# Optimization experiments

Measured on AMD Instinct MI355X. Metric: run time of the kernel, lower is better.

The kernel has to match this reference:

```python
import jax, jax.numpy as jnp
from jax import lax
import numpy as np

T, B, NIN, H, NOUT = 256, 64, 512, 512, 512


def _lstm_dir(x, w_ih, w_hh, b_ih, b_hh, reverse):
    # x: [T,B,NIN]; w_ih: [4H,NIN]; w_hh: [4H,H]
    xg = jnp.einsum('tbi,gi->tbg', x, w_ih) + b_ih + b_hh  # [T,B,4H]
    if reverse:
        xg = xg[::-1]
    h0 = jnp.zeros((x.shape[1], w_hh.shape[1]), x.dtype)

    def step(carry, g):
        h, c = carry
        g = g + h @ w_hh.T
        i, f, gg, o = jnp.split(g, 4, axis=-1)  # PyTorch gate order i,f,g,o
        i = jax.nn.sigmoid(i)
        f = jax.nn.sigmoid(f)
        gg = jnp.tanh(gg)
        o = jax.nn.sigmoid(o)
        c = f * c + i * gg
        h = o * jnp.tanh(c)
        return (h, c), h

    _, hs = lax.scan(step, (h0, h0), xg)
    if reverse:
        hs = hs[::-1]
    return hs  # [T,B,H]


def setup_inputs() -> dict:
    key = jax.random.key(0)
    ks = jax.random.split(key, 12)
    s_in = 1.0 / np.sqrt(H)
    u = lambda k, shape: jax.random.uniform(k, shape, jnp.float32, -s_in, s_in)
    return {
        'x': jax.random.normal(ks[0], (T, B, NIN), jnp.float32),
        'w_ih_f': u(ks[1], (4 * H, NIN)),
        'w_hh_f': u(ks[2], (4 * H, H)),
        'b_ih_f': u(ks[3], (4 * H,)),
        'b_hh_f': u(ks[4], (4 * H,)),
        'w_ih_b': u(ks[5], (4 * H, NIN)),
        'w_hh_b': u(ks[6], (4 * H, H)),
        'b_ih_b': u(ks[7], (4 * H,)),
        'b_hh_b': u(ks[8], (4 * H,)),
        'fc_w': u(ks[9], (NOUT, 2 * H)),
        'fc_b': u(ks[10], (NOUT,)),
    }


def reference(x, w_ih_f, w_hh_f, b_ih_f, b_hh_f, w_ih_b, w_hh_b, b_ih_b, b_hh_b, fc_w, fc_b):
    h_f = _lstm_dir(x, w_ih_f, w_hh_f, b_ih_f, b_hh_f, reverse=False)
    h_b = _lstm_dir(x, w_ih_b, w_hh_b, b_ih_b, b_hh_b, reverse=True)
    h = jnp.concatenate([h_f, h_b], axis=-1)  # [T,B,2H]
    out = jnp.einsum('tbh,oh->tbo', h, fc_w) + fc_b  # fused linear over T*B rows
    return out
```

## Files before the change

kernel.cpp:

```cpp
#include <hip/hip_runtime.h>

typedef unsigned short u16;
typedef short v8s __attribute__((ext_vector_type(8)));
typedef float v4f __attribute__((ext_vector_type(4)));

#define TT 256
#define BB 64
#define HH 512
#define G4 2048
#define MTB 16384

static __device__ __forceinline__ float bf2f(u16 u) {
    unsigned int x = ((unsigned int)u) << 16;
    union { unsigned int i; float f; } c; c.i = x; return c.f;
}
static __device__ __forceinline__ u16 f2bf(float f) {
    union { float f; unsigned int i; } c; c.f = f;
    unsigned int u = c.i;
    u += 0x7fffu + ((u >> 16) & 1u);
    return (u16)(u >> 16);
}

__global__ __launch_bounds__(256) void cvt_bf16(const float* __restrict__ src,
                                                u16* __restrict__ dst, int n) {
    int i = blockIdx.x * blockDim.x + threadIdx.x;
    int stride = gridDim.x * blockDim.x;
    for (int j = i * 4; j < n; j += stride * 4) {
        float4 v = *reinterpret_cast<const float4*>(src + j);
        ushort4 o;
        o.x = f2bf(v.x); o.y = f2bf(v.y); o.z = f2bf(v.z); o.w = f2bf(v.w);
        *reinterpret_cast<ushort4*>(dst + j) = o;
    }
}

template<bool OUT_BF16, bool BIAS_M>
__global__ __launch_bounds__(256) void gemm_bt(const u16* __restrict__ A,
                                               const u16* __restrict__ Bm,
                                               void* __restrict__ Cv,
                                               const float* __restrict__ bias1,
                                               const float* __restrict__ bias2,
                                               int M, int N, int K) {
    __shared__ u16 lds_a[128 * 64];
    __shared__ u16 lds_b[128 * 64];
    const int tid = threadIdx.x, lane = tid & 63;
    const int m0 = blockIdx.y * 128, n0 = blockIdx.x * 128;
    const int wid = tid >> 6, wm = wid >> 1, wn = wid & 1;
    v4f acc[4][4] = {};

    const int srow  = tid >> 3;
    const int skoff = (tid & 7) * 8;
    const u16* Ag = A + (size_t)(m0 + srow) * K + skoff;
    const u16* Bg = Bm + (size_t)(n0 + srow) * K + skoff;
    u16* la = lds_a + srow * 64 + skoff;
    u16* lb = lds_b + srow * 64 + skoff;

    for (int k0 = 0; k0 < K; k0 += 64) {
        #pragma unroll
        for (int q = 0; q < 4; ++q) {
            *reinterpret_cast<v8s*>(la + q * 32 * 64) =
                *reinterpret_cast<const v8s*>(Ag + (size_t)q * 32 * K + k0);
            *reinterpret_cast<v8s*>(lb + q * 32 * 64) =
                *reinterpret_cast<const v8s*>(Bg + (size_t)q * 32 * K + k0);
        }
        __syncthreads();
        #pragma unroll
        for (int kk = 0; kk < 2; ++kk) {
            v8s af[4], bfr[4];
            #pragma unroll
            for (int i = 0; i < 4; ++i)
                af[i] = *reinterpret_cast<const v8s*>(
                    lds_a + (wm * 64 + i * 16 + (lane & 15)) * 64 + kk * 32 + (lane >> 4) * 8);
            #pragma unroll
            for (int i = 0; i < 4; ++i)
                bfr[i] = *reinterpret_cast<const v8s*>(
                    lds_b + (wn * 64 + i * 16 + (lane & 15)) * 64 + kk * 32 + (lane >> 4) * 8);
            #pragma unroll
            for (int i = 0; i < 4; ++i)
                #pragma unroll
                for (int j = 0; j < 4; ++j)
                    acc[i][j] = __builtin_amdgcn_mfma_f32_16x16x32_bf16(af[i], bfr[j], acc[i][j], 0, 0, 0);
        }
        __syncthreads();
    }
    #pragma unroll
    for (int i = 0; i < 4; ++i) {
        #pragma unroll
        for (int j = 0; j < 4; ++j) {
            #pragma unroll
            for (int r = 0; r < 4; ++r) {
                int m = m0 + wm * 64 + i * 16 + (lane >> 4) * 4 + r;
                int n = n0 + wn * 64 + j * 16 + (lane & 15);
                float v = acc[i][j][r];
                if (BIAS_M) { v += bias1[m]; if (bias2) v += bias2[m]; }
                else        { v += bias1[n]; }
                if (OUT_BF16) ((u16*)Cv)[(size_t)m * N + n] = f2bf(v);
                else          ((float*)Cv)[(size_t)m * N + n] = v;
            }
        }
    }
}

static __device__ __forceinline__ float sigm(float x) { return 1.f / (1.f + __expf(-x)); }
static __device__ __forceinline__ float tanh_(float x) { return 2.f / (1.f + __expf(-2.f * x)) - 1.f; }

__global__ __launch_bounds__(256, 2) void lstm_persist(
    const u16* __restrict__ w_hh,
    const u16* __restrict__ xgT,
    u16* __restrict__ h_all,
    unsigned* __restrict__ flags)
{
    __shared__ u16 wlds[4 * 16 * 64 * 8];
    const int bx = blockIdx.x;
    const int d = bx >> 5, cg = bx & 31;
    const int lane = threadIdx.x & 63, nf = threadIdx.x >> 6;
    const int lrow = lane & 15, lk = lane >> 4;
    const int b = nf * 16 + lrow;

    {
        const int G = nf;
        const u16* wrow = w_hh + ((size_t)d * G4 + G * HH + cg * 16 + lrow) * HH + lk * 8;
        #pragma unroll
        for (int kk = 0; kk < 16; ++kk)
            *reinterpret_cast<v8s*>(&wlds[((G * 16 + kk) * 64 + lane) * 8]) =
                *reinterpret_cast<const v8s*>(wrow + kk * 32);
    }
    __syncthreads();

    float c[4] = {0.f, 0.f, 0.f, 0.f};
    float xg[4][4];
    unsigned* fl = flags + (d * 4 + nf) * 32;

    {
        const int t0 = d ? (TT - 1) : 0;
        const u16* xgb = xgT + (size_t)d * G4 * MTB + (size_t)t0 * BB + b;
        #pragma unroll
        for (int G = 0; G < 4; ++G)
            #pragma unroll
            for (int r = 0; r < 4; ++r)
                xg[G][r] = bf2f(xgb[(size_t)(G * HH + cg * 16 + lk * 4 + r) * MTB]);
    }

    for (int s = 0; s < TT; ++s) {
        const int t = d ? (TT - 1 - s) : s;
        v4f acc[4] = {};
        if (s > 0) {
            v8s af0[4][4];
            #pragma unroll
            for (int G = 0; G < 4; ++G)
                #pragma unroll
                for (int kk = 0; kk < 4; ++kk)
                    af0[G][kk] = *reinterpret_cast<const v8s*>(
                        &wlds[((G * 16 + kk) * 64 + lane) * 8]);
            const unsigned tgt = (unsigned)s;
            while (true) {
                unsigned fv = __hip_atomic_load(&fl[lane & 31],
                                                __ATOMIC_RELAXED, __HIP_MEMORY_SCOPE_AGENT);
                if (__all((int)(fv >= tgt))) break;
            }
            asm volatile("" ::: "memory");
            const int tprev = d ? (t + 1) : (t - 1);
            const u16* hp = h_all + ((size_t)tprev * BB + b) * 1024 + d * HH + lk * 8;
            v8s bf_[16];
            #pragma unroll
            for (int kk = 0; kk < 16; ++kk) {
                union { unsigned long long w[2]; v8s v; } u;
                const u16* p = hp + kk * 32;
                u.w[0] = __hip_atomic_load((const unsigned long long*)p,
                                           __ATOMIC_RELAXED, __HIP_MEMORY_SCOPE_AGENT);
                u.w[1] = __hip_atomic_load((const unsigned long long*)(p + 4),
                                           __ATOMIC_RELAXED, __HIP_MEMORY_SCOPE_AGENT);
                bf_[kk] = u.v;
            }
            #pragma unroll
            for (int kk = 0; kk < 4; ++kk)
                #pragma unroll
                for (int G = 0; G < 4; ++G)
                    acc[G] = __builtin_amdgcn_mfma_f32_16x16x32_bf16(af0[G][kk], bf_[kk], acc[G], 0, 0, 0);
            #pragma unroll
            for (int kk = 4; kk < 16; ++kk)
                #pragma unroll
                for (int G = 0; G < 4; ++G) {
                    v8s af = *reinterpret_cast<const v8s*>(
                        &wlds[((G * 16 + kk) * 64 + lane) * 8]);
                    acc[G] = __builtin_amdgcn_mfma_f32_16x16x32_bf16(af, bf_[kk], acc[G], 0, 0, 0);
                }
        }
        ushort4 hout;
        #pragma unroll
        for (int r = 0; r < 4; ++r) {
            float pi = acc[0][r] + xg[0][r];
            float pf = acc[1][r] + xg[1][r];
            float pg = acc[2][r] + xg[2][r];
            float po = acc[3][r] + xg[3][r];
            float iv = sigm(pi), fv = sigm(pf), gv = tanh_(pg), ov = sigm(po);
            float cc = fv * c[r] + iv * gv;
            c[r] = cc;
            ((u16*)&hout)[r] = f2bf(ov * tanh_(cc));
        }
        union { ushort4 v; unsigned long long q; } hu; hu.v = hout;
        __hip_atomic_store((unsigned long long*)(
                h_all + ((size_t)t * BB + b) * 1024 + d * HH + cg * 16 + lk * 4),
            hu.q, __ATOMIC_RELAXED, __HIP_MEMORY_SCOPE_AGENT);
        asm volatile("s_waitcnt vmcnt(0)" ::: "memory");
        if (lane == 0)
            __hip_atomic_store(&fl[cg], (unsigned)(s + 1),
                               __ATOMIC_RELAXED, __HIP_MEMORY_SCOPE_AGENT);
        if (s + 1 < TT) {
            const int tn = d ? (TT - 2 - s) : (s + 1);
            const u16* xgb = xgT + (size_t)d * G4 * MTB + (size_t)tn * BB + b;
            #pragma unroll
            for (int G = 0; G < 4; ++G)
                #pragma unroll
                for (int r = 0; r < 4; ++r)
                    xg[G][r] = bf2f(xgb[(size_t)(G * HH + cg * 16 + lk * 4 + r) * MTB]);
        }
    }
}

extern "C" void kernel_launch(void* const* d_in, const int* in_sizes, int n_in,
                              void* d_out, int out_size, void* d_ws, size_t ws_size,
                              hipStream_t stream) {
    const float* x    = (const float*)d_in[0];
    const float* wihf = (const float*)d_in[1];
    const float* whhf = (const float*)d_in[2];
    const float* bihf = (const float*)d_in[3];
    const float* bhhf = (const float*)d_in[4];
    const float* wihb = (const float*)d_in[5];
    const float* whhb = (const float*)d_in[6];
    const float* bihb = (const float*)d_in[7];
    const float* bhhb = (const float*)d_in[8];
    const float* fcw  = (const float*)d_in[9];
    const float* fcb  = (const float*)d_in[10];

    char* ws = (char*)d_ws;
    size_t off = 0;
    auto alloc = [&](size_t bytes) {
        off = (off + 255) & ~(size_t)255;
        char* p = ws + off; off += bytes; return p;
    };
    u16* x_bf    = (u16*)alloc((size_t)MTB * 512 * 2);
    u16* wih_bf  = (u16*)alloc((size_t)2 * G4 * 512 * 2);
    u16* whh_bf  = (u16*)alloc((size_t)2 * G4 * 512 * 2);
    u16* fcw_bf  = (u16*)alloc((size_t)512 * 1024 * 2);
    u16* xgT     = (u16*)alloc((size_t)2 * G4 * MTB * 2);
    u16* h_all   = (u16*)alloc((size_t)MTB * 1024 * 2);
    unsigned* flags = (unsigned*)alloc(2 * 4 * 32 * sizeof(unsigned));
    (void)ws_size;

    cvt_bf16<<<1024, 256, 0, stream>>>(x, x_bf, MTB * 512);
    cvt_bf16<<<256, 256, 0, stream>>>(wihf, wih_bf, G4 * 512);
    cvt_bf16<<<256, 256, 0, stream>>>(wihb, wih_bf + (size_t)G4 * 512, G4 * 512);
    cvt_bf16<<<256, 256, 0, stream>>>(whhf, whh_bf, G4 * 512);
    cvt_bf16<<<256, 256, 0, stream>>>(whhb, whh_bf + (size_t)G4 * 512, G4 * 512);
    cvt_bf16<<<128, 256, 0, stream>>>(fcw, fcw_bf, 512 * 1024);

    gemm_bt<true, true><<<dim3(MTB / 128, G4 / 128), 256, 0, stream>>>(
        wih_bf, x_bf, xgT, bihf, bhhf, G4, MTB, 512);
    gemm_bt<true, true><<<dim3(MTB / 128, G4 / 128), 256, 0, stream>>>(
        wih_bf + (size_t)G4 * 512, x_bf, xgT + (size_t)G4 * MTB, bihb, bhhb, G4, MTB, 512);

    hipMemsetAsync(flags, 0, 2 * 4 * 32 * sizeof(unsigned), stream);
    lstm_persist<<<64, 256, 0, stream>>>(whh_bf, xgT, h_all, flags);

    gemm_bt<false, false><<<dim3(512 / 128, MTB / 128), 256, 0, stream>>>(
        h_all, fcw_bf, d_out, fcb, nullptr, MTB, 512, 1024);
}
```

Measured before the change: 1.525 ms.

## Replace flag-based sync with timestep-tagged hidden state words in LSTM recurrence

Drops the separate per-group progress flags and the store-wait-flag sequence. Each bf16 hidden value is now written into a 32-bit word whose upper half holds the timestep, so consumers poll the data itself until every tag matches. This removes a full memory round trip and the vmcnt wait from every recurrent step. In exchange the hidden buffer doubles in size, needs a 0xFF memset beforehand, and the FC GEMM must unpack tagged words when loading A. The MFMA chain is also split into two accumulators to shorten the dependency chain.

```diff
diff --git a/kernel.cpp b/kernel.cpp
--- a/kernel.cpp
+++ b/kernel.cpp
@@ -1,6 +1,8 @@
 #include <hip/hip_runtime.h>
 
 typedef unsigned short u16;
+typedef unsigned int u32;
+typedef unsigned long long u64;
 typedef short v8s __attribute__((ext_vector_type(8)));
 typedef float v4f __attribute__((ext_vector_type(4)));
 
@@ -11,12 +13,12 @@
 #define MTB 16384
 
 static __device__ __forceinline__ float bf2f(u16 u) {
-    unsigned int x = ((unsigned int)u) << 16;
-    union { unsigned int i; float f; } c; c.i = x; return c.f;
+    u32 x = ((u32)u) << 16;
+    union { u32 i; float f; } c; c.i = x; return c.f;
 }
 static __device__ __forceinline__ u16 f2bf(float f) {
-    union { float f; unsigned int i; } c; c.f = f;
-    unsigned int u = c.i;
+    union { float f; u32 i; } c; c.f = f;
+    u32 u = c.i;
     u += 0x7fffu + ((u >> 16) & 1u);
     return (u16)(u >> 16);
 }
@@ -33,8 +35,8 @@
     }
 }
 
-template<bool OUT_BF16, bool BIAS_M>
-__global__ __launch_bounds__(256) void gemm_bt(const u16* __restrict__ A,
+template<bool OUT_BF16, bool BIAS_M, bool A_TAG>
+__global__ __launch_bounds__(256) void gemm_bt(const void* __restrict__ Av,
                                                const u16* __restrict__ Bm,
                                                void* __restrict__ Cv,
                                                const float* __restrict__ bias1,
@@ -49,7 +51,8 @@
 
     const int srow  = tid >> 3;
     const int skoff = (tid & 7) * 8;
-    const u16* Ag = A + (size_t)(m0 + srow) * K + skoff;
+    const u16* Ag  = A_TAG ? nullptr : (const u16*)Av + (size_t)(m0 + srow) * K + skoff;
+    const u32* Agt = A_TAG ? (const u32*)Av + (size_t)(m0 + srow) * K + skoff : nullptr;
     const u16* Bg = Bm + (size_t)(n0 + srow) * K + skoff;
     u16* la = lds_a + srow * 64 + skoff;
     u16* lb = lds_b + srow * 64 + skoff;
@@ -57,8 +60,19 @@
     for (int k0 = 0; k0 < K; k0 += 64) {
         #pragma unroll
         for (int q = 0; q < 4; ++q) {
-            *reinterpret_cast<v8s*>(la + q * 32 * 64) =
-                *reinterpret_cast<const v8s*>(Ag + (size_t)q * 32 * K + k0);
+            if (A_TAG) {
+                uint4 u0 = *reinterpret_cast<const uint4*>(Agt + (size_t)q * 32 * K + k0);
+                uint4 u1 = *reinterpret_cast<const uint4*>(Agt + (size_t)q * 32 * K + k0 + 4);
+                union { u32 w[4]; v8s v; } P;
+                P.w[0] = (u0.x & 0xFFFFu) | (u0.y << 16);
+                P.w[1] = (u0.z & 0xFFFFu) | (u0.w << 16);
+                P.w[2] = (u1.x & 0xFFFFu) | (u1.y << 16);
+                P.w[3] = (u1.z & 0xFFFFu) | (u1.w << 16);
+                *reinterpret_cast<v8s*>(la + q * 32 * 64) = P.v;
+            } else {
+                *reinterpret_cast<v8s*>(la + q * 32 * 64) =
+                    *reinterpret_cast<const v8s*>(Ag + (size_t)q * 32 * K + k0);
+            }
             *reinterpret_cast<v8s*>(lb + q * 32 * 64) =
                 *reinterpret_cast<const v8s*>(Bg + (size_t)q * 32 * K + k0);
         }
@@ -106,8 +120,7 @@
 __global__ __launch_bounds__(256, 2) void lstm_persist(
     const u16* __restrict__ w_hh,
     const u16* __restrict__ xgT,
-    u16* __restrict__ h_all,
-    unsigned* __restrict__ flags)
+    u32* __restrict__ hx)
 {
     __shared__ u16 wlds[4 * 16 * 64 * 8];
     const int bx = blockIdx.x;
@@ -128,7 +141,6 @@
 
     float c[4] = {0.f, 0.f, 0.f, 0.f};
     float xg[4][4];
-    unsigned* fl = flags + (d * 4 + nf) * 32;
 
     {
         const int t0 = d ? (TT - 1) : 0;
@@ -142,50 +154,47 @@
 
     for (int s = 0; s < TT; ++s) {
         const int t = d ? (TT - 1 - s) : s;
-        v4f acc[4] = {};
+        v4f acc[4] = {}, acc2[4] = {};
         if (s > 0) {
-            v8s af0[4][4];
+            const int tprev = d ? (t + 1) : (t - 1);
+            const u64 expv = (u64)((u32)tprev << 16);
+            const u32* hpc = hx + ((size_t)tprev * BB + b) * 1024 + d * HH + lk * 8;
+            v8s bf_[16];
+            while (true) {
+                u64 bad = 0;
+                #pragma unroll
+                for (int kk = 0; kk < 16; ++kk) {
+                    const u64* p = (const u64*)(hpc + kk * 32);
+                    u64 q0 = __hip_atomic_load(p + 0, __ATOMIC_RELAXED, __HIP_MEMORY_SCOPE_AGENT);
+                    u64 q1 = __hip_atomic_load(p + 1, __ATOMIC_RELAXED, __HIP_MEMORY_SCOPE_AGENT);
+                    u64 q2 = __hip_atomic_load(p + 2, __ATOMIC_RELAXED, __HIP_MEMORY_SCOPE_AGENT);
+                    u64 q3 = __hip_atomic_load(p + 3, __ATOMIC_RELAXED, __HIP_MEMORY_SCOPE_AGENT);
+                    bad |= ((q0 ^ expv) | (q1 ^ expv) | (q2 ^ expv) | (q3 ^ expv))
+                           & 0x00000000FFFF0000ULL;
+                    union { u32 w[4]; v8s v; } P;
+                    P.w[0] = ((u32)q0 & 0xFFFFu) | ((u32)(q0 >> 32) << 16);
+                    P.w[1] = ((u32)q1 & 0xFFFFu) | ((u32)(q1 >> 32) << 16);
+                    P.w[2] = ((u32)q2 & 0xFFFFu) | ((u32)(q2 >> 32) << 16);
+                    P.w[3] = ((u32)q3 & 0xFFFFu) | ((u32)(q3 >> 32) << 16);
+                    bf_[kk] = P.v;
+                }
+                if (__all(bad == 0)) break;
+            }
+            #pragma unroll
+            for (int kk = 0; kk < 16; kk += 2)
+                #pragma unroll
+                for (int G = 0; G < 4; ++G) {
+                    v8s af0 = *reinterpret_cast<const v8s*>(&wlds[((G * 16 + kk) * 64 + lane) * 8]);
+                    v8s af1 = *reinterpret_cast<const v8s*>(&wlds[((G * 16 + kk + 1) * 64 + lane) * 8]);
+                    acc[G]  = __builtin_amdgcn_mfma_f32_16x16x32_bf16(af0, bf_[kk],     acc[G],  0, 0, 0);
+                    acc2[G] = __builtin_amdgcn_mfma_f32_16x16x32_bf16(af1, bf_[kk + 1], acc2[G], 0, 0, 0);
+                }
             #pragma unroll
             for (int G = 0; G < 4; ++G)
-                #pragma unroll
-                for (int kk = 0; kk < 4; ++kk)
-                    af0[G][kk] = *reinterpret_cast<const v8s*>(
-                        &wlds[((G * 16 + kk) * 64 + lane) * 8]);
-            const unsigned tgt = (unsigned)s;
-            while (true) {
-                unsigned fv = __hip_atomic_load(&fl[lane & 31],
-                                                __ATOMIC_RELAXED, __HIP_MEMORY_SCOPE_AGENT);
-                if (__all((int)(fv >= tgt))) break;
-            }
-            asm volatile("" ::: "memory");
-            const int tprev = d ? (t + 1) : (t - 1);
-            const u16* hp = h_all + ((size_t)tprev * BB + b) * 1024 + d * HH + lk * 8;
-            v8s bf_[16];
-            #pragma unroll
-            for (int kk = 0; kk < 16; ++kk) {
-                union { unsigned long long w[2]; v8s v; } u;
-                const u16* p = hp + kk * 32;
-                u.w[0] = __hip_atomic_load((const unsigned long long*)p,
-                                           __ATOMIC_RELAXED, __HIP_MEMORY_SCOPE_AGENT);
-                u.w[1] = __hip_atomic_load((const unsigned long long*)(p + 4),
-                                           __ATOMIC_RELAXED, __HIP_MEMORY_SCOPE_AGENT);
-                bf_[kk] = u.v;
-            }
-            #pragma unroll
-            for (int kk = 0; kk < 4; ++kk)
-                #pragma unroll
-                for (int G = 0; G < 4; ++G)
-                    acc[G] = __builtin_amdgcn_mfma_f32_16x16x32_bf16(af0[G][kk], bf_[kk], acc[G], 0, 0, 0);
-            #pragma unroll
-            for (int kk = 4; kk < 16; ++kk)
-                #pragma unroll
-                for (int G = 0; G < 4; ++G) {
-                    v8s af = *reinterpret_cast<const v8s*>(
-                        &wlds[((G * 16 + kk) * 64 + lane) * 8]);
-                    acc[G] = __builtin_amdgcn_mfma_f32_16x16x32_bf16(af, bf_[kk], acc[G], 0, 0, 0);
-                }
-        }
-        ushort4 hout;
+                acc[G] += acc2[G];
+        }
+        const u32 tg = (u32)t << 16;
+        u32 hw[4];
         #pragma unroll
         for (int r = 0; r < 4; ++r) {
             float pi = acc[0][r] + xg[0][r];
@@ -195,16 +204,13 @@
             float iv = sigm(pi), fv = sigm(pf), gv = tanh_(pg), ov = sigm(po);
             float cc = fv * c[r] + iv * gv;
             c[r] = cc;
-            ((u16*)&hout)[r] = f2bf(ov * tanh_(cc));
-        }
-        union { ushort4 v; unsigned long long q; } hu; hu.v = hout;
-        __hip_atomic_store((unsigned long long*)(
-                h_all + ((size_t)t * BB + b) * 1024 + d * HH + cg * 16 + lk * 4),
-            hu.q, __ATOMIC_RELAXED, __HIP_MEMORY_SCOPE_AGENT);
-        asm volatile("s_waitcnt vmcnt(0)" ::: "memory");
-        if (lane == 0)
-            __hip_atomic_store(&fl[cg], (unsigned)(s + 1),
-                               __ATOMIC_RELAXED, __HIP_MEMORY_SCOPE_AGENT);
+            hw[r] = tg | (u32)f2bf(ov * tanh_(cc));
+        }
+        u64 w0 = (u64)hw[0] | ((u64)hw[1] << 32);
+        u64 w1 = (u64)hw[2] | ((u64)hw[3] << 32);
+        u64* hp = (u64*)(hx + ((size_t)t * BB + b) * 1024 + d * HH + cg * 16 + lk * 4);
+        __hip_atomic_store(hp,     w0, __ATOMIC_RELAXED, __HIP_MEMORY_SCOPE_AGENT);
+        __hip_atomic_store(hp + 1, w1, __ATOMIC_RELAXED, __HIP_MEMORY_SCOPE_AGENT);
         if (s + 1 < TT) {
             const int tn = d ? (TT - 2 - s) : (s + 1);
             const u16* xgb = xgT + (size_t)d * G4 * MTB + (size_t)tn * BB + b;
@@ -243,8 +249,7 @@
     u16* whh_bf  = (u16*)alloc((size_t)2 * G4 * 512 * 2);
     u16* fcw_bf  = (u16*)alloc((size_t)512 * 1024 * 2);
     u16* xgT     = (u16*)alloc((size_t)2 * G4 * MTB * 2);
-    u16* h_all   = (u16*)alloc((size_t)MTB * 1024 * 2);
-    unsigned* flags = (unsigned*)alloc(2 * 4 * 32 * sizeof(unsigned));
+    u32* hx      = (u32*)alloc((size_t)MTB * 1024 * 4);
     (void)ws_size;
 
     cvt_bf16<<<1024, 256, 0, stream>>>(x, x_bf, MTB * 512);
@@ -254,14 +259,15 @@
     cvt_bf16<<<256, 256, 0, stream>>>(whhb, whh_bf + (size_t)G4 * 512, G4 * 512);
     cvt_bf16<<<128, 256, 0, stream>>>(fcw, fcw_bf, 512 * 1024);
 
-    gemm_bt<true, true><<<dim3(MTB / 128, G4 / 128), 256, 0, stream>>>(
+    hipMemsetAsync(hx, 0xFF, (size_t)MTB * 1024 * 4, stream);
+
+    gemm_bt<true, true, false><<<dim3(MTB / 128, G4 / 128), 256, 0, stream>>>(
         wih_bf, x_bf, xgT, bihf, bhhf, G4, MTB, 512);
-    gemm_bt<true, true><<<dim3(MTB / 128, G4 / 128), 256, 0, stream>>>(
+    gemm_bt<true, true, false><<<dim3(MTB / 128, G4 / 128), 256, 0, stream>>>(
         wih_bf + (size_t)G4 * 512, x_bf, xgT + (size_t)G4 * MTB, bihb, bhhb, G4, MTB, 512);
 
-    hipMemsetAsync(flags, 0, 2 * 4 * 32 * sizeof(unsigned), stream);
-    lstm_persist<<<64, 256, 0, stream>>>(whh_bf, xgT, h_all, flags);
-
-    gemm_bt<false, false><<<dim3(512 / 128, MTB / 128), 256, 0, stream>>>(
-        h_all, fcw_bf, d_out, fcb, nullptr, MTB, 512, 1024);
-}
+    lstm_persist<<<64, 256, 0, stream>>>(whh_bf, xgT, hx);
+
+    gemm_bt<false, false, true><<<dim3(512 / 128, MTB / 128), 256, 0, stream>>>(
+        hx, fcw_bf, d_out, fcb, nullptr, MTB, 512, 1024);
+}
```

New measurement: 3.709 ms. +143.2%, slower.
